# Performance work log

Hardware: AMD Instinct MI355X
Metric: run time of the kernel (lower is better)

Reference implementation:

```python
import jax, jax.numpy as jnp
import numpy as np

D_IN = 768      # inp_dim
NH = 8          # head_num
HD = 96         # head_dim
HID = NH * HD   # 768
UP = 2 * D_IN   # p_factor[0]=2.0 -> 1536
FUSED = 2 * NH + 3 * HID  # 2320
KER = 4
CS = 64         # chunk_size
CAP = 15.0      # gate_soft_cap
EPS = 1e-6


def _ln(x, w, b):
    m = jnp.mean(x, -1, keepdims=True)
    v = jnp.mean((x - m) ** 2, -1, keepdims=True)
    return (x - m) / jnp.sqrt(v + EPS) * w + b


def setup_inputs() -> dict:
    key = jax.random.key(0)
    ks = jax.random.split(key, 10)
    B, S = 2, 4096
    def lin(k, fin, fout):
        return (jax.random.normal(k, (fin, fout), jnp.float32) / np.sqrt(fin)).astype(jnp.float32)
    return {
        "x": jax.random.normal(ks[0], (B, S, D_IN), jnp.float32),
        "ln_in_w": jnp.ones((D_IN,), jnp.float32), "ln_in_b": jnp.zeros((D_IN,), jnp.float32),
        "ln_hid_w": jnp.ones((HID,), jnp.float32), "ln_hid_b": jnp.zeros((HID,), jnp.float32),
        "up_l_w": lin(ks[1], D_IN, UP), "up_l_b": jnp.zeros((UP,), jnp.float32),
        "up_r_w": lin(ks[2], D_IN, HID), "up_r_b": jnp.zeros((HID,), jnp.float32),
        "down_w": lin(ks[3], HID, D_IN), "down_b": jnp.zeros((D_IN,), jnp.float32),
        "conv_w": (jax.random.normal(ks[4], (KER,), jnp.float32) * 0.5).astype(jnp.float32),
        "conv_b": jnp.zeros((), jnp.float32),
        "skip_w": lin(ks[5], UP, HID), "skip_b": jnp.zeros((HID,), jnp.float32),
        "fused_w": lin(ks[6], UP, FUSED), "fused_b": jnp.zeros((FUSED,), jnp.float32),
        "wo_w": lin(ks[7], UP, HID), "wo_b": jnp.zeros((HID,), jnp.float32),
    }


def reference(x, ln_in_w, ln_in_b, ln_hid_w, ln_hid_b, up_l_w, up_l_b, up_r_w, up_r_b,
              down_w, down_b, conv_w, conv_b, skip_w, skip_b, fused_w, fused_b, wo_w, wo_b):
    B, S, _ = x.shape
    soft_cap = lambda t: CAP * jnp.tanh(t / CAP)

    x_n = _ln(x, ln_in_w, ln_in_b)
    x_t = x_n @ up_l_w + up_l_b          # [B,S,UP]
    r_t = x_n @ up_r_w + up_r_b          # [B,S,HID]

    # causal conv: single shared (1,1,KER) kernel, depthwise across UP channels
    xp = jnp.pad(x_t, ((0, 0), (KER - 1, 0), (0, 0)))
    x_c = conv_b + sum(conv_w[j] * xp[:, j:j + S, :] for j in range(KER))
    x_c = jax.nn.silu(x_c)

    x_skip = x_c @ skip_w + skip_b
    proj = x_c @ fused_w + fused_b
    i_pre = soft_cap(proj[..., :NH])
    f_pre = soft_cap(proj[..., NH:2 * NH])
    q, k, v = jnp.split(proj[..., 2 * NH:], 3, axis=-1)
    o = jax.nn.sigmoid(x_t @ wo_w + wo_b)

    resh = lambda t: t.reshape(B, S, NH, HD).transpose(0, 2, 1, 3)  # [B,NH,S,HD]
    q = resh(q)
    k = resh(k) / np.sqrt(HD)
    v = resh(v)

    i_g = i_pre.transpose(0, 2, 1)  # [B,NH,S]
    f_g = f_pre.transpose(0, 2, 1)
    mx = jnp.maximum(f_g, i_g)
    i_g = jnp.exp(i_g - mx)
    f_g = jnp.exp(f_g - mx)

    NC = S // CS
    qc = q.reshape(B, NH, NC, CS, HD)
    kc = k.reshape(B, NH, NC, CS, HD)
    vc = v.reshape(B, NH, NC, CS, HD)
    ic = i_g.reshape(B, NH, NC, CS)
    fc = f_g.reshape(B, NH, NC, CS)

    lf = jnp.cumsum(jnp.log(fc + 1e-8), -1)          # [B,NH,NC,CS]
    f_cumul = jnp.exp(lf - lf[..., -1:])
    wC = f_cumul * ic
    # inter-chunk states; final_forget = exp(lf[-1]-lf[-1]) == 1 exactly -> exclusive cumsum
    C_contrib = jnp.einsum('bncl,bncld,bncle->bncde', wC, vc, kc)  # v-outer-k
    n_contrib = jnp.einsum('bncl,bncld->bncd', wC, kc)
    C_init = jnp.concatenate([jnp.zeros_like(C_contrib[:, :, :1]),
                              jnp.cumsum(C_contrib, axis=2)[:, :, :-1]], axis=2)
    n_init = jnp.concatenate([jnp.zeros_like(n_contrib[:, :, :1]),
                              jnp.cumsum(n_contrib, axis=2)[:, :, :-1]], axis=2)

    # intra-chunk, strictly-causal (j < i)
    mask = jnp.tril(jnp.ones((CS, CS), bool), -1)
    dl = lf[..., :, None] - lf[..., None, :]
    w = jnp.where(mask, ic[..., None, :] * jnp.exp(jnp.where(mask, dl, 0.0)), 0.0)
    scores = jnp.einsum('bncid,bncjd->bncij', qc, kc)
    attn = jax.nn.softmax(jnp.where(mask, scores, -1e30), axis=-1)
    attn = jnp.where(mask, attn, 0.0)  # pos 0 row -> all zeros

    h_intra = jnp.einsum('bncij,bncjd->bncid', attn * w, vc)
    n_intra = jnp.einsum('bncij,bncjd->bncid', w, kc)
    h_init = jnp.einsum('bncde,bncie->bncid', C_init, qc)

    total_n = n_init[..., None, :] + n_intra
    denom = jnp.maximum(jnp.sum(total_n * qc, -1, keepdims=True), 1.0)
    h = (h_init + h_intra) / denom                    # [B,NH,NC,CS,HD]

    h = h.reshape(B, NH, S, HD).transpose(0, 2, 1, 3).reshape(B, S, HID)
    h = o * h
    out = _ln(h, ln_hid_w, ln_hid_b) + x_skip
    out = out * jax.nn.silu(r_t)
    out = out @ down_w + down_b
    return out + x
```

## Files before the change

kernel.cpp:

```cpp
#include <hip/hip_runtime.h>
#include <hip/hip_bf16.h>
#include <math.h>

#define D_IN  768
#define NHD   8
#define HDIM  96
#define HID   768
#define UPD   1536
#define FUSED 2320
#define KER   4
#define CS    64
#define NCH   64
#define SB    4096
#define BB    2
#define NROW  (BB*SB)
#define NCHUNK (BB*NHD*NCH)

using u16   = unsigned short;
using frag8 = __attribute__((ext_vector_type(8))) short;
using f32x4 = __attribute__((ext_vector_type(4))) float;

#define O_WUPL   0
#define O_WUPR   1769472
#define O_WSKIP  2359296
#define O_WFUS   3538944
#define O_WWO    9142272
#define O_WDOWN  10321920
#define O_RT     10911744
#define O_XSKIP  17203200
#define O_LF     23494656
#define O_IC     23560192
#define O_WC     23625728
#define O_NC     23691264
#define O_XN     23789568
#define O_XT     33226752
#define O_XTS    45809664
#define O_PROJ   23789568
#define O_CC     23789568
#define O_H      33226752
#define O_OUT1   39518208

__device__ __forceinline__ void gld_lds16u(const u16* g, u16* l) {
    __builtin_amdgcn_global_load_lds(
        (const __attribute__((address_space(1))) void*)g,
        (__attribute__((address_space(3))) void*)l, 16, 0, 0);
}

__device__ __forceinline__ void split3u(float f, unsigned &H, unsigned &M, unsigned &L) {
    unsigned u = __float_as_uint(f);
    unsigned hr = (u + 0x7fffu + ((u >> 16) & 1u)) & 0xffff0000u;
    H = hr;
    float rm = f - __uint_as_float(hr);
    unsigned mr = __float_as_uint(rm) & 0xffff0000u;
    M = mr;
    float rl = rm - __uint_as_float(mr);
    L = __float_as_uint(rl) & 0xffff0000u;
}

__global__ __launch_bounds__(256) void tpose_split(
    const float* __restrict__ w, u16* __restrict__ tH, u16* __restrict__ tM,
    u16* __restrict__ tL, int K, int N)
{
    __shared__ float tile[64][65];
    int k0 = blockIdx.x * 64, n0 = blockIdx.y * 64;
    int t = threadIdx.x;
    int c = t & 63, r4 = t >> 6;
    #pragma unroll
    for (int it = 0; it < 16; ++it) {
        int r = r4 + it * 4;
        int n = n0 + c;
        tile[r][c] = (n < N) ? w[(size_t)(k0 + r) * N + n] : 0.f;
    }
    __syncthreads();
    #pragma unroll
    for (int it = 0; it < 16; ++it) {
        int nn = r4 + it * 4;
        float v = tile[c][nn];
        unsigned H, M, L;
        split3u(v, H, M, L);
        size_t idx = (size_t)(n0 + nn) * K + k0 + c;
        tH[idx] = (u16)(H >> 16);
        tM[idx] = (u16)(M >> 16);
        if (tL) tL[idx] = (u16)(L >> 16);
    }
}

__global__ __launch_bounds__(256) void ln_in_split(
    const float* __restrict__ x, const float* __restrict__ w,
    const float* __restrict__ b, u16* __restrict__ oH,
    u16* __restrict__ oM, u16* __restrict__ oL)
{
    int row = blockIdx.x;
    size_t base = (size_t)row * D_IN;
    int c0 = threadIdx.x, c1 = threadIdx.x + 256, c2 = threadIdx.x + 512;
    float v0 = x[base + c0], v1 = x[base + c1], v2 = x[base + c2];
    float s = v0 + v1 + v2;
    float ss = v0*v0 + v1*v1 + v2*v2;
    for (int off = 32; off; off >>= 1) { s += __shfl_xor(s, off); ss += __shfl_xor(ss, off); }
    __shared__ float red[8];
    int wid = threadIdx.x >> 6;
    if ((threadIdx.x & 63) == 0) { red[wid] = s; red[4 + wid] = ss; }
    __syncthreads();
    s = red[0] + red[1] + red[2] + red[3];
    ss = red[4] + red[5] + red[6] + red[7];
    float mean = s * (1.f / D_IN);
    float var = ss * (1.f / D_IN) - mean * mean;
    float inv = rsqrtf(var + 1e-6f);
    float r0 = (v0 - mean) * inv * w[c0] + b[c0];
    float r1 = (v1 - mean) * inv * w[c1] + b[c1];
    float r2 = (v2 - mean) * inv * w[c2] + b[c2];
    unsigned H, M, L;
    split3u(r0, H, M, L); oH[base+c0]=(u16)(H>>16); oM[base+c0]=(u16)(M>>16); oL[base+c0]=(u16)(L>>16);
    split3u(r1, H, M, L); oH[base+c1]=(u16)(H>>16); oM[base+c1]=(u16)(M>>16); oL[base+c1]=(u16)(L>>16);
    split3u(r2, H, M, L); oH[base+c2]=(u16)(H>>16); oM[base+c2]=(u16)(M>>16); oL[base+c2]=(u16)(L>>16);
}

template<int NT, int NTH>
__global__ __launch_bounds__(NTH) void gemm_sp(
    const u16* __restrict__ aH, const u16* __restrict__ aM, const u16* __restrict__ aL,
    const u16* __restrict__ bH, const u16* __restrict__ bM, const u16* __restrict__ bL,
    const float* __restrict__ bias, const float* __restrict__ resid,
    float* __restrict__ C, u16* __restrict__ cH, u16* __restrict__ cM,
    int N, int K, int act)
{
    constexpr int BM = (NT == 6) ? 256 : 128;
    __shared__ u16 AHM[2][BM * 64];
    __shared__ u16 BHM[2][128 * 64];
    __shared__ u16 ALp[(NT == 6) ? 2 : 1][(NT == 6) ? 128 * 64 : 8];
    __shared__ u16 BLp[(NT == 6) ? 2 : 1][(NT == 6) ? 64 * 64 : 8];

    int t = threadIdx.x;
    int wave = t >> 6, lane = t & 63;
    int lin = blockIdx.y * gridDim.x + blockIdx.x;
    int cpx = (gridDim.x * gridDim.y) >> 3;
    int sw  = (lin & 7) * cpx + (lin >> 3);
    int bx = sw % gridDim.x, by = sw / gridDim.x;
    int m0 = by * BM, n0 = bx * 128;

    int wm = (wave >> 1) * 64, wn = (wave & 1) * 64;
    f32x4 acc[4][4] = {};

    int l7 = lane & 7, l8 = lane >> 3;
    int lc = l7 ^ l8;
    int lane15 = lane & 15, rsel = lane >> 4;
    int pH = (rsel ^ l7) * 8;
    int pM = ((4 | rsel) ^ l7) * 8;
    int aLrow = (lane15 >> 1) * 64 + (((((lane & 1) << 2) | rsel) ^ (lane15 >> 1)) * 8);
    int wslot = wave;

    auto stage = [&](int buf, int k0) {
        if constexpr (NT == 6) {
            #pragma unroll
            for (int j = 0; j < 4; ++j) {
                int g = j * 8 + wslot;
                int r = g * 8 + l8;
                const u16* src = (lc >= 4 ? aM : aH) + (size_t)(m0 + r) * K + k0 + (lc & 3) * 8;
                gld_lds16u(src, &AHM[buf][g * 512 + lane * 8]);
            }
            #pragma unroll
            for (int j = 0; j < 2; ++j) {
                int g = j * 8 + wslot;
                int r = g * 8 + l8;
                const u16* src = (lc >= 4 ? bM : bH) + (size_t)(n0 + r) * K + k0 + (lc & 3) * 8;
                gld_lds16u(src, &BHM[buf][g * 512 + lane * 8]);
            }
            #pragma unroll
            for (int j = 0; j < 2; ++j) {
                int g = j * 8 + wslot;
                int R = g * 8 + l8;
                int rr = 2 * R + (lc >> 2);
                const u16* src = aL + (size_t)(m0 + rr) * K + k0 + (lc & 3) * 8;
                gld_lds16u(src, &ALp[buf][g * 512 + lane * 8]);
            }
            {
                int g = wslot;
                int R = g * 8 + l8;
                int rr = 2 * R + (lc >> 2);
                const u16* src = bL + (size_t)(n0 + rr) * K + k0 + (lc & 3) * 8;
                gld_lds16u(src, &BLp[buf][g * 512 + lane * 8]);
            }
        } else {
            #pragma unroll
            for (int j = 0; j < 4; ++j) {
                int g = j * 4 + wslot;
                int r = g * 8 + l8;
                const u16* src = (lc >= 4 ? aM : aH) + (size_t)(m0 + r) * K + k0 + (lc & 3) * 8;
                gld_lds16u(src, &AHM[buf][g * 512 + lane * 8]);
            }
            #pragma unroll
            for (int j = 0; j < 4; ++j) {
                int g = j * 4 + wslot;
                int r = g * 8 + l8;
                const u16* src = (lc >= 4 ? bM : bH) + (size_t)(n0 + r) * K + k0 + (lc & 3) * 8;
                gld_lds16u(src, &BHM[buf][g * 512 + lane * 8]);
            }
        }
    };

    auto compute = [&](int buf) {
        frag8 ah[4], am[4], al[(NT == 6) ? 4 : 1];
        #pragma unroll
        for (int mi = 0; mi < 4; ++mi) {
            int rr = wm + mi * 16 + lane15;
            const u16* bp = &AHM[buf][rr * 64];
            ah[mi] = *(const frag8*)&bp[pH];
            am[mi] = *(const frag8*)&bp[pM];
            if constexpr (NT == 6)
                al[mi] = *(const frag8*)&ALp[buf][(wm >> 1) * 64 + mi * 512 + aLrow];
        }
        #pragma unroll
        for (int ni = 0; ni < 4; ++ni) {
            int rb = wn + ni * 16 + lane15;
            const u16* bp = &BHM[buf][rb * 64];
            frag8 bh = *(const frag8*)&bp[pH];
            frag8 bm = *(const frag8*)&bp[pM];
            if constexpr (NT == 6) {
                frag8 bl = *(const frag8*)&BLp[buf][(wn >> 1) * 64 + ni * 512 + aLrow];
                #pragma unroll
                for (int mi = 0; mi < 4; ++mi) {
                    acc[mi][ni] = __builtin_amdgcn_mfma_f32_16x16x32_bf16(ah[mi], bm, acc[mi][ni], 0, 0, 0);
                    acc[mi][ni] = __builtin_amdgcn_mfma_f32_16x16x32_bf16(am[mi], bh, acc[mi][ni], 0, 0, 0);
                    acc[mi][ni] = __builtin_amdgcn_mfma_f32_16x16x32_bf16(ah[mi], bl, acc[mi][ni], 0, 0, 0);
                    acc[mi][ni] = __builtin_amdgcn_mfma_f32_16x16x32_bf16(al[mi], bh, acc[mi][ni], 0, 0, 0);
                    acc[mi][ni] = __builtin_amdgcn_mfma_f32_16x16x32_bf16(am[mi], bm, acc[mi][ni], 0, 0, 0);
                    acc[mi][ni] = __builtin_amdgcn_mfma_f32_16x16x32_bf16(ah[mi], bh, acc[mi][ni], 0, 0, 0);
                }
            } else {
                #pragma unroll
                for (int mi = 0; mi < 4; ++mi) {
                    acc[mi][ni] = __builtin_amdgcn_mfma_f32_16x16x32_bf16(ah[mi], bm, acc[mi][ni], 0, 0, 0);
                    acc[mi][ni] = __builtin_amdgcn_mfma_f32_16x16x32_bf16(am[mi], bh, acc[mi][ni], 0, 0, 0);
                    acc[mi][ni] = __builtin_amdgcn_mfma_f32_16x16x32_bf16(ah[mi], bh, acc[mi][ni], 0, 0, 0);
                }
            }
        }
    };

    int ns = K >> 5;
    stage(0, 0);
    asm volatile("" ::: "memory");
    int cur = 0;
    for (int s = 0; s < ns - 1; ++s) {
        stage(cur ^ 1, (s + 1) * 32);
        if constexpr (NT == 6) asm volatile("s_waitcnt vmcnt(9)" ::: "memory");
        else                   asm volatile("s_waitcnt vmcnt(8)" ::: "memory");
        __builtin_amdgcn_sched_barrier(0);
        __builtin_amdgcn_s_barrier();
        compute(cur);
        __builtin_amdgcn_s_barrier();
        cur ^= 1;
    }
    asm volatile("s_waitcnt vmcnt(0)" ::: "memory");
    __builtin_amdgcn_sched_barrier(0);
    __builtin_amdgcn_s_barrier();
    compute(cur);

    const bool dosplit = (cH != nullptr);
    #pragma unroll
    for (int ni = 0; ni < 4; ++ni) {
        int ncol = n0 + wn + ni * 16 + (lane & 15);
        if (ncol >= N) continue;
        float bs = bias[ncol];
        #pragma unroll
        for (int mi = 0; mi < 4; ++mi) {
            #pragma unroll
            for (int r = 0; r < 4; ++r) {
                int mrow = m0 + wm + mi * 16 + (lane >> 4) * 4 + r;
                float val = acc[mi][ni][r] + bs;
                if (act == 1) val = 1.f / (1.f + expf(-val));
                if (resid) val += resid[(size_t)mrow * N + ncol];
                C[(size_t)mrow * N + ncol] = val;
                if (dosplit) {
                    unsigned H, M, L;
                    split3u(val, H, M, L);
                    cH[(size_t)mrow * N + ncol] = (u16)(H >> 16);
                    cM[(size_t)mrow * N + ncol] = (u16)(M >> 16);
                }
            }
        }
    }
}

__global__ void conv_split(const float* __restrict__ xt, const float* __restrict__ cw,
                           const float* __restrict__ cb, u16* __restrict__ xcH,
                           u16* __restrict__ xcM, u16* __restrict__ xcL)
{
    size_t idx = (size_t)blockIdx.x * blockDim.x + threadIdx.x;
    if (idx >= (size_t)NROW * UPD) return;
    int ch = idx % UPD;
    int s = (int)((idx / UPD) % SB);
    int b = (int)(idx / ((size_t)UPD * SB));
    float acc = cb[0];
    #pragma unroll
    for (int j = 0; j < KER; ++j) {
        int sj = s - (KER - 1) + j;
        if (sj >= 0) acc += cw[j] * xt[((size_t)b * SB + sj) * UPD + ch];
    }
    float v = acc / (1.f + expf(-acc));
    unsigned H, M, L;
    split3u(v, H, M, L);
    xcH[idx] = (u16)(H >> 16);
    xcM[idx] = (u16)(M >> 16);
    xcL[idx] = (u16)(L >> 16);
}

__global__ __launch_bounds__(64) void gates_kernel(
    const float* __restrict__ proj, float* __restrict__ lf,
    float* __restrict__ ic, float* __restrict__ wC)
{
    int cid = blockIdx.x;
    int l = threadIdx.x;
    int b = cid >> 9;
    int nh = (cid >> 6) & 7;
    int c = cid & 63;
    int s = c * CS + l;
    size_t row = ((size_t)b * SB + s) * FUSED;
    float ip = proj[row + nh];
    float fp = proj[row + NHD + nh];
    ip = 15.f * tanhf(ip * (1.f / 15.f));
    fp = 15.f * tanhf(fp * (1.f / 15.f));
    float mx = fmaxf(ip, fp);
    float ig = expf(ip - mx);
    float fg = expf(fp - mx);
    float v = logf(fg + 1e-8f);
    for (int off = 1; off < 64; off <<= 1) {
        float u = __shfl_up(v, off);
        if (l >= off) v += u;
    }
    float last = __shfl(v, 63);
    lf[cid * CS + l] = v;
    ic[cid * CS + l] = ig;
    wC[cid * CS + l] = expf(v - last) * ig;
}

__global__ void repack_kernel(const float* __restrict__ proj, float* __restrict__ q,
                              float* __restrict__ k, float* __restrict__ v)
{
    size_t idx = (size_t)blockIdx.x * blockDim.x + threadIdx.x;
    if (idx >= (size_t)BB * NHD * NCH * CS * HDIM) return;
    int d = idx % HDIM; size_t r1 = idx / HDIM;
    int l = r1 % CS; r1 /= CS;
    int c = r1 % NCH; r1 /= NCH;
    int nh = r1 % NHD; int b = (int)(r1 / NHD);
    size_t row = ((size_t)b * SB + c * CS + l) * FUSED + 2 * NHD + nh * HDIM + d;
    q[idx] = proj[row];
    k[idx] = proj[row + HID] * 0.10206207261596577f;
    v[idx] = proj[row + 2 * HID];
}

__global__ __launch_bounds__(256) void chunk_outer_kernel(
    const float* __restrict__ k, const float* __restrict__ v,
    const float* __restrict__ wC, float* __restrict__ Cc, float* __restrict__ nc)
{
    __shared__ float kL[CS * HDIM], vL[CS * HDIM], wL[CS];
    int cid = blockIdx.x, t = threadIdx.x;
    const float* kg = k + (size_t)cid * CS * HDIM;
    const float* vg = v + (size_t)cid * CS * HDIM;
    for (int idx = t; idx < CS * HDIM; idx += 256) { kL[idx] = kg[idx]; vL[idx] = vg[idx]; }
    if (t < CS) wL[t] = wC[cid * CS + t];
    __syncthreads();
    int eb = t >> 3;
    int db = t & 7;
    float4 acc[3][3];
    #pragma unroll
    for (int e2 = 0; e2 < 3; ++e2)
        #pragma unroll
        for (int x = 0; x < 3; ++x) acc[e2][x] = make_float4(0.f, 0.f, 0.f, 0.f);
    for (int l = 0; l < CS; ++l) {
        float w = wL[l];
        float wk[3];
        #pragma unroll
        for (int e2 = 0; e2 < 3; ++e2) wk[e2] = w * kL[l * HDIM + 3 * eb + e2];
        const float* vr = &vL[l * HDIM + 12 * db];
        float4 vv[3];
        #pragma unroll
        for (int x = 0; x < 3; ++x) vv[x] = *(const float4*)(vr + 4 * x);
        #pragma unroll
        for (int e2 = 0; e2 < 3; ++e2)
            #pragma unroll
            for (int x = 0; x < 3; ++x) {
                acc[e2][x].x += wk[e2] * vv[x].x;
                acc[e2][x].y += wk[e2] * vv[x].y;
                acc[e2][x].z += wk[e2] * vv[x].z;
                acc[e2][x].w += wk[e2] * vv[x].w;
            }
    }
    float* Cb = Cc + (size_t)cid * HDIM * HDIM;
    #pragma unroll
    for (int e2 = 0; e2 < 3; ++e2)
        #pragma unroll
        for (int x = 0; x < 3; ++x)
            *(float4*)&Cb[(size_t)(3 * eb + e2) * HDIM + 12 * db + 4 * x] = acc[e2][x];
    if (t < HDIM) {
        float acc2 = 0.f;
        for (int l = 0; l < CS; ++l) acc2 += wL[l] * kL[l * HDIM + t];
        nc[(size_t)cid * HDIM + t] = acc2;
    }
}

__global__ void scan_kernel(float* __restrict__ Cc, float* __restrict__ nc)
{
    int gid = blockIdx.x * blockDim.x + threadIdx.x;
    const int NCE = BB * NHD * HDIM * HDIM;
    if (gid < NCE) {
        int bh = gid / (HDIM * HDIM);
        int ent = gid % (HDIM * HDIM);
        float run = 0.f;
        float* base = Cc + (size_t)bh * NCH * HDIM * HDIM + ent;
        for (int c = 0; c < NCH; ++c) {
            float tv = base[(size_t)c * HDIM * HDIM];
            base[(size_t)c * HDIM * HDIM] = run;
            run += tv;
        }
    } else {
        int g2 = gid - NCE;
        if (g2 < BB * NHD * HDIM) {
            int bh = g2 / HDIM, ent = g2 % HDIM;
            float run = 0.f;
            float* base = nc + (size_t)bh * NCH * HDIM + ent;
            for (int c = 0; c < NCH; ++c) {
                float tv = base[c * HDIM];
                base[c * HDIM] = run;
                run += tv;
            }
        }
    }
}

__global__ __launch_bounds__(256) void attn_kernel(
    const float* __restrict__ q, const float* __restrict__ k, const float* __restrict__ v,
    const float* __restrict__ lf, const float* __restrict__ ic,
    const float* __restrict__ CiT, const float* __restrict__ ni,
    float* __restrict__ hout)
{
    __shared__ float qL[64 * 100];
    __shared__ float kL[64 * 100];
    __shared__ float lfL[64], icL[64], niL[96], dinvL[64];
    int cid = blockIdx.x, t = threadIdx.x;
    int b = cid >> 9, nh = (cid >> 6) & 7, c = cid & 63;
    const float* qg = q + (size_t)cid * (CS * HDIM);
    const float* kg = k + (size_t)cid * (CS * HDIM);
    const float* vg = v + (size_t)cid * (CS * HDIM);
    const float4* qg4 = (const float4*)qg;
    const float4* kg4 = (const float4*)kg;
    #pragma unroll
    for (int it = 0; it < 6; ++it) {
        int idx = t + it * 256;
        int row = idx / 24, col = (idx % 24) * 4;
        *(float4*)&qL[row * 100 + col] = qg4[idx];
        *(float4*)&kL[row * 100 + col] = kg4[idx];
    }
    if (t < 64) { lfL[t] = lf[cid * CS + t]; icL[t] = ic[cid * CS + t]; }
    else if (t < 160) { niL[t - 64] = ni[(size_t)cid * HDIM + (t - 64)]; }
    __syncthreads();

    int i = t >> 2, g = t & 3;
    const float* qrow = qL + i * 100;
    float sc[16];
    #pragma unroll
    for (int jj = 0; jj < 16; ++jj) sc[jj] = 0.f;
    for (int d4 = 0; d4 < 24; ++d4) {
        float4 qv = *(const float4*)(qrow + 4 * d4);
        #pragma unroll
        for (int jj = 0; jj < 16; ++jj) {
            float4 kv = *(const float4*)(kL + (g + 4 * jj) * 100 + 4 * d4);
            sc[jj] += qv.x * kv.x + qv.y * kv.y + qv.z * kv.z + qv.w * kv.w;
        }
    }
    float lfi = lfL[i];
    float wv[16];
    #pragma unroll
    for (int jj = 0; jj < 16; ++jj) {
        int j = g + 4 * jj;
        wv[jj] = (j < i) ? icL[j] * expf(lfi - lfL[j]) : 0.f;
    }
    float den = 0.f;
    #pragma unroll
    for (int jj = 0; jj < 16; ++jj) den += wv[jj] * sc[jj];
    #pragma unroll
    for (int dd = 0; dd < 24; ++dd) {
        int d = 24 * g + dd;
        den += niL[d] * qrow[d];
    }
    float m = -1e30f;
    #pragma unroll
    for (int jj = 0; jj < 16; ++jj) { int j = g + 4 * jj; if (j < i) m = fmaxf(m, sc[jj]); }
    m = fmaxf(m, __shfl_xor(m, 1)); m = fmaxf(m, __shfl_xor(m, 2));
    float p = 0.f;
    #pragma unroll
    for (int jj = 0; jj < 16; ++jj) {
        int j = g + 4 * jj;
        sc[jj] = (j < i) ? expf(sc[jj] - m) : 0.f;
        p += sc[jj];
    }
    p += __shfl_xor(p, 1); p += __shfl_xor(p, 2);
    float pinv = (p > 0.f) ? 1.f / p : 0.f;
    __syncthreads();
    float* awL = kL;
    #pragma unroll
    for (int jj = 0; jj < 16; ++jj) {
        int j = g + 4 * jj;
        awL[i * 68 + j] = sc[jj] * pinv * wv[jj];
    }
    den += __shfl_xor(den, 1); den += __shfl_xor(den, 2);
    if ((t & 3) == 0) dinvL[i] = 1.f / fmaxf(den, 1.f);
    __syncthreads();

    int i0 = (t >> 3) << 1, db = (t & 7) * 12;
    float4 h4[2][3];
    #pragma unroll
    for (int r = 0; r < 2; ++r)
        #pragma unroll
        for (int x = 0; x < 3; ++x) h4[r][x] = make_float4(0.f, 0.f, 0.f, 0.f);
    const float* vb = vg + db;
    const float* aw0 = awL + i0 * 68;
    for (int j = 0; j < 64; ++j) {
        float a0 = aw0[j];
        float a1 = aw0[68 + j];
        const float4* vr = (const float4*)(vb + j * HDIM);
        #pragma unroll
        for (int x = 0; x < 3; ++x) {
            float4 vv = vr[x];
            h4[0][x].x += a0 * vv.x; h4[0][x].y += a0 * vv.y;
            h4[0][x].z += a0 * vv.z; h4[0][x].w += a0 * vv.w;
            h4[1][x].x += a1 * vv.x; h4[1][x].y += a1 * vv.y;
            h4[1][x].z += a1 * vv.z; h4[1][x].w += a1 * vv.w;
        }
    }
    const float* Cb = CiT + (size_t)cid * (HDIM * HDIM) + db;
    const float* qr0 = qL + i0 * 100;
    const float* qr1 = qr0 + 100;
    for (int e = 0; e < 96; ++e) {
        float q0 = qr0[e], q1 = qr1[e];
        const float4* cr = (const float4*)(Cb + e * HDIM);
        #pragma unroll
        for (int x = 0; x < 3; ++x) {
            float4 cv = cr[x];
            h4[0][x].x += q0 * cv.x; h4[0][x].y += q0 * cv.y;
            h4[0][x].z += q0 * cv.z; h4[0][x].w += q0 * cv.w;
            h4[1][x].x += q1 * cv.x; h4[1][x].y += q1 * cv.y;
            h4[1][x].z += q1 * cv.z; h4[1][x].w += q1 * cv.w;
        }
    }
    float di0 = dinvL[i0], di1 = dinvL[i0 + 1];
    int s0 = c * CS + i0;
    float4* hr0 = (float4*)(hout + (((size_t)b * SB + s0) * NHD + nh) * HDIM + db);
    float4* hr1 = (float4*)(hout + (((size_t)b * SB + s0 + 1) * NHD + nh) * HDIM + db);
    #pragma unroll
    for (int x = 0; x < 3; ++x) {
        float4 h0 = h4[0][x], h1 = h4[1][x];
        h0.x *= di0; h0.y *= di0; h0.z *= di0; h0.w *= di0;
        h1.x *= di1; h1.y *= di1; h1.z *= di1; h1.w *= di1;
        hr0[x] = h0;
        hr1[x] = h1;
    }
}

__global__ __launch_bounds__(256) void ln_hid_split(
    const float* __restrict__ h, const float* __restrict__ o,
    const float* __restrict__ xskip, const float* __restrict__ rt,
    const float* __restrict__ w, const float* __restrict__ bb,
    u16* __restrict__ oH, u16* __restrict__ oM)
{
    int row = blockIdx.x;
    size_t base = (size_t)row * HID;
    int c0 = threadIdx.x, c1 = threadIdx.x + 256, c2 = threadIdx.x + 512;
    float v0 = o[base + c0] * h[base + c0];
    float v1 = o[base + c1] * h[base + c1];
    float v2 = o[base + c2] * h[base + c2];
    float s = v0 + v1 + v2;
    float ss = v0*v0 + v1*v1 + v2*v2;
    for (int off = 32; off; off >>= 1) { s += __shfl_xor(s, off); ss += __shfl_xor(ss, off); }
    __shared__ float red[8];
    int wid = threadIdx.x >> 6;
    if ((threadIdx.x & 63) == 0) { red[wid] = s; red[4 + wid] = ss; }
    __syncthreads();
    s = red[0] + red[1] + red[2] + red[3];
    ss = red[4] + red[5] + red[6] + red[7];
    float mean = s * (1.f / HID);
    float var = ss * (1.f / HID) - mean * mean;
    float inv = rsqrtf(var + 1e-6f);
    float g0 = rt[base + c0], g1 = rt[base + c1], g2 = rt[base + c2];
    float r0 = ((v0 - mean) * inv * w[c0] + bb[c0] + xskip[base + c0]) * (g0 / (1.f + expf(-g0)));
    float r1 = ((v1 - mean) * inv * w[c1] + bb[c1] + xskip[base + c1]) * (g1 / (1.f + expf(-g1)));
    float r2 = ((v2 - mean) * inv * w[c2] + bb[c2] + xskip[base + c2]) * (g2 / (1.f + expf(-g2)));
    unsigned H, M, L;
    split3u(r0, H, M, L); oH[base+c0]=(u16)(H>>16); oM[base+c0]=(u16)(M>>16);
    split3u(r1, H, M, L); oH[base+c1]=(u16)(H>>16); oM[base+c1]=(u16)(M>>16);
    split3u(r2, H, M, L); oH[base+c2]=(u16)(H>>16); oM[base+c2]=(u16)(M>>16);
}

extern "C" void kernel_launch(void* const* d_in, const int* in_sizes, int n_in,
                              void* d_out, int out_size, void* d_ws, size_t ws_size,
                              hipStream_t stream)
{
    const float* x       = (const float*)d_in[0];
    const float* ln_in_w = (const float*)d_in[1];
    const float* ln_in_b = (const float*)d_in[2];
    const float* ln_hid_w= (const float*)d_in[3];
    const float* ln_hid_b= (const float*)d_in[4];
    const float* up_l_w  = (const float*)d_in[5];
    const float* up_l_b  = (const float*)d_in[6];
    const float* up_r_w  = (const float*)d_in[7];
    const float* up_r_b  = (const float*)d_in[8];
    const float* down_w  = (const float*)d_in[9];
    const float* down_b  = (const float*)d_in[10];
    const float* conv_w  = (const float*)d_in[11];
    const float* conv_b  = (const float*)d_in[12];
    const float* skip_w  = (const float*)d_in[13];
    const float* skip_b  = (const float*)d_in[14];
    const float* fused_w = (const float*)d_in[15];
    const float* fused_b = (const float*)d_in[16];
    const float* wo_w    = (const float*)d_in[17];
    const float* wo_b    = (const float*)d_in[18];
    float* out = (float*)d_out;

    float* ws = (float*)d_ws;
    u16* wuplH = (u16*)(ws + O_WUPL);  u16* wuplM = wuplH + 1179648; u16* wuplL = wuplM + 1179648;
    u16* wuprH = (u16*)(ws + O_WUPR);  u16* wuprM = wuprH + 589824;
    u16* wskpH = (u16*)(ws + O_WSKIP); u16* wskpM = wskpH + 1179648;
    u16* wfusH = (u16*)(ws + O_WFUS);  u16* wfusM = wfusH + 3735552; u16* wfusL = wfusM + 3735552;
    u16* wwoH  = (u16*)(ws + O_WWO);   u16* wwoM  = wwoH  + 1179648;
    u16* wdwnH = (u16*)(ws + O_WDOWN); u16* wdwnM = wdwnH + 589824;
    float* rt    = ws + O_RT;
    float* xskip = ws + O_XSKIP;
    float* lf    = ws + O_LF;
    float* ic    = ws + O_IC;
    float* wC    = ws + O_WC;
    float* nc    = ws + O_NC;
    u16* xnH = (u16*)(ws + O_XN);  u16* xnM = xnH + 6291456; u16* xnL = xnM + 6291456;
    float* xt = ws + O_XT;
    u16* xtH = (u16*)(ws + O_XTS); u16* xtM = xtH + 12582912;
    u16* xcH = (u16*)(ws + O_XTS); u16* xcM = xcH + 12582912; u16* xcL = xcM + 12582912;
    float* proj = ws + O_PROJ;
    float* q = ws + O_XTS;
    float* k = ws + O_XTS + 6291456;
    float* v = ws + O_XTS + 12582912;
    float* Cc = ws + O_CC;
    float* h  = ws + O_H;
    u16* out1H = (u16*)(ws + O_OUT1); u16* out1M = out1H + 6291456;
    float* o = (float*)d_out;

    tpose_split<<<dim3(12, 24), 256, 0, stream>>>(up_l_w, wuplH, wuplM, wuplL, 768, 1536);
    tpose_split<<<dim3(12, 12), 256, 0, stream>>>(up_r_w, wuprH, wuprM, nullptr, 768, 768);
    tpose_split<<<dim3(24, 12), 256, 0, stream>>>(skip_w, wskpH, wskpM, nullptr, 1536, 768);
    tpose_split<<<dim3(24, 38), 256, 0, stream>>>(fused_w, wfusH, wfusM, wfusL, 1536, 2320);
    tpose_split<<<dim3(24, 12), 256, 0, stream>>>(wo_w, wwoH, wwoM, nullptr, 1536, 768);
    tpose_split<<<dim3(12, 12), 256, 0, stream>>>(down_w, wdwnH, wdwnM, nullptr, 768, 768);
    ln_in_split<<<NROW, 256, 0, stream>>>(x, ln_in_w, ln_in_b, xnH, xnM, xnL);
    gemm_sp<6,512><<<dim3(12, 32), 512, 0, stream>>>(xnH, xnM, xnL, wuplH, wuplM, wuplL,
        up_l_b, nullptr, xt, xtH, xtM, UPD, D_IN, 0);
    gemm_sp<3,256><<<dim3(6, 64), 256, 0, stream>>>(xnH, xnM, nullptr, wuprH, wuprM, nullptr,
        up_r_b, nullptr, rt, nullptr, nullptr, HID, D_IN, 0);
    gemm_sp<3,256><<<dim3(6, 64), 256, 0, stream>>>(xtH, xtM, nullptr, wwoH, wwoM, nullptr,
        wo_b, nullptr, o, nullptr, nullptr, HID, UPD, 1);
    {
        size_t tot = (size_t)NROW * UPD;
        conv_split<<<(unsigned)((tot + 255) / 256), 256, 0, stream>>>(xt, conv_w, conv_b, xcH, xcM, xcL);
    }
    gemm_sp<3,256><<<dim3(6, 64), 256, 0, stream>>>(xcH, xcM, nullptr, wskpH, wskpM, nullptr,
        skip_b, nullptr, xskip, nullptr, nullptr, HID, UPD, 0);
    gemm_sp<6,512><<<dim3(19, 32), 512, 0, stream>>>(xcH, xcM, xcL, wfusH, wfusM, wfusL,
        fused_b, nullptr, proj, nullptr, nullptr, FUSED, UPD, 0);
    gates_kernel<<<NCHUNK, 64, 0, stream>>>(proj, lf, ic, wC);
    {
        size_t tot = (size_t)BB * NHD * NCH * CS * HDIM;
        repack_kernel<<<(unsigned)((tot + 255) / 256), 256, 0, stream>>>(proj, q, k, v);
    }
    chunk_outer_kernel<<<NCHUNK, 256, 0, stream>>>(k, v, wC, Cc, nc);
    {
        int tot = BB * NHD * HDIM * HDIM + BB * NHD * HDIM;
        scan_kernel<<<(tot + 255) / 256, 256, 0, stream>>>(Cc, nc);
    }
    attn_kernel<<<NCHUNK, 256, 0, stream>>>(q, k, v, lf, ic, Cc, nc, h);
    ln_hid_split<<<NROW, 256, 0, stream>>>(h, o, xskip, rt, ln_hid_w, ln_hid_b, out1H, out1M);
    gemm_sp<3,256><<<dim3(6, 64), 256, 0, stream>>>(out1H, out1M, nullptr, wdwnH, wdwnM, nullptr,
        down_b, x, out, nullptr, nullptr, D_IN, HID, 0);
}
```

Measured before the change: 1.129 ms.

## Merge sibling GEMMs into mixed-precision launches and drop q/k/v repack kernel

Concatenates up_l and up_r weights into one GEMM launch, and fused and skip weights into another. Tiles in the second region skip the low-order split terms and run 3 MFMAs instead of 6, and their results go to a separate output buffer. The repack kernel is removed, and chunk_outer and attn now read q/k/v directly from proj with strided rows, applying the k scale inline. This cuts launch count and a full copy of q/k/v through memory, in exchange for uncoalesced strided reads from proj and a more complex GEMM epilogue.

```diff
diff --git a/kernel.cpp b/kernel.cpp
--- a/kernel.cpp
+++ b/kernel.cpp
@@ -15,17 +15,16 @@
 #define BB    2
 #define NROW  (BB*SB)
 #define NCHUNK (BB*NHD*NCH)
+#define KSCALE 0.10206207261596577f
 
 using u16   = unsigned short;
 using frag8 = __attribute__((ext_vector_type(8))) short;
 using f32x4 = __attribute__((ext_vector_type(4))) float;
 
-#define O_WUPL   0
-#define O_WUPR   1769472
-#define O_WSKIP  2359296
-#define O_WFUS   3538944
-#define O_WWO    9142272
-#define O_WDOWN  10321920
+#define O_WUP    0
+#define O_WWO    2359296
+#define O_WDOWN  3538944
+#define O_WFUS   4128768
 #define O_RT     10911744
 #define O_XSKIP  17203200
 #define O_LF     23494656
@@ -36,8 +35,8 @@
 #define O_XT     33226752
 #define O_XTS    45809664
 #define O_PROJ   23789568
-#define O_CC     23789568
-#define O_H      33226752
+#define O_CC     45809664
+#define O_H      55246848
 #define O_OUT1   39518208
 
 __device__ __forceinline__ void gld_lds16u(const u16* g, u16* l) {
@@ -121,7 +120,8 @@
     const u16* __restrict__ bH, const u16* __restrict__ bM, const u16* __restrict__ bL,
     const float* __restrict__ bias, const float* __restrict__ resid,
     float* __restrict__ C, u16* __restrict__ cH, u16* __restrict__ cM,
-    int N, int K, int act)
+    int ldC, int N1, int NP1, float* __restrict__ C2, const float* __restrict__ bias2,
+    int K, int act)
 {
     constexpr int BM = (NT == 6) ? 256 : 128;
     __shared__ u16 AHM[2][BM * 64];
@@ -136,6 +136,7 @@
     int sw  = (lin & 7) * cpx + (lin >> 3);
     int bx = sw % gridDim.x, by = sw / gridDim.x;
     int m0 = by * BM, n0 = bx * 128;
+    const bool lact = (NT == 6) && (n0 < NP1);
 
     int wm = (wave >> 1) * 64, wn = (wave & 1) * 64;
     f32x4 acc[4][4] = {};
@@ -164,20 +165,22 @@
                 const u16* src = (lc >= 4 ? bM : bH) + (size_t)(n0 + r) * K + k0 + (lc & 3) * 8;
                 gld_lds16u(src, &BHM[buf][g * 512 + lane * 8]);
             }
-            #pragma unroll
-            for (int j = 0; j < 2; ++j) {
-                int g = j * 8 + wslot;
-                int R = g * 8 + l8;
-                int rr = 2 * R + (lc >> 2);
-                const u16* src = aL + (size_t)(m0 + rr) * K + k0 + (lc & 3) * 8;
-                gld_lds16u(src, &ALp[buf][g * 512 + lane * 8]);
-            }
-            {
-                int g = wslot;
-                int R = g * 8 + l8;
-                int rr = 2 * R + (lc >> 2);
-                const u16* src = bL + (size_t)(n0 + rr) * K + k0 + (lc & 3) * 8;
-                gld_lds16u(src, &BLp[buf][g * 512 + lane * 8]);
+            if (lact) {
+                #pragma unroll
+                for (int j = 0; j < 2; ++j) {
+                    int g = j * 8 + wslot;
+                    int R = g * 8 + l8;
+                    int rr = 2 * R + (lc >> 2);
+                    const u16* src = aL + (size_t)(m0 + rr) * K + k0 + (lc & 3) * 8;
+                    gld_lds16u(src, &ALp[buf][g * 512 + lane * 8]);
+                }
+                {
+                    int g = wslot;
+                    int R = g * 8 + l8;
+                    int rr = 2 * R + (lc >> 2);
+                    const u16* src = bL + (size_t)(n0 + rr) * K + k0 + (lc & 3) * 8;
+                    gld_lds16u(src, &BLp[buf][g * 512 + lane * 8]);
+                }
             }
         } else {
             #pragma unroll
@@ -206,7 +209,7 @@
             ah[mi] = *(const frag8*)&bp[pH];
             am[mi] = *(const frag8*)&bp[pM];
             if constexpr (NT == 6)
-                al[mi] = *(const frag8*)&ALp[buf][(wm >> 1) * 64 + mi * 512 + aLrow];
+                if (lact) al[mi] = *(const frag8*)&ALp[buf][(wm >> 1) * 64 + mi * 512 + aLrow];
         }
         #pragma unroll
         for (int ni = 0; ni < 4; ++ni) {
@@ -215,15 +218,24 @@
             frag8 bh = *(const frag8*)&bp[pH];
             frag8 bm = *(const frag8*)&bp[pM];
             if constexpr (NT == 6) {
-                frag8 bl = *(const frag8*)&BLp[buf][(wn >> 1) * 64 + ni * 512 + aLrow];
-                #pragma unroll
-                for (int mi = 0; mi < 4; ++mi) {
-                    acc[mi][ni] = __builtin_amdgcn_mfma_f32_16x16x32_bf16(ah[mi], bm, acc[mi][ni], 0, 0, 0);
-                    acc[mi][ni] = __builtin_amdgcn_mfma_f32_16x16x32_bf16(am[mi], bh, acc[mi][ni], 0, 0, 0);
-                    acc[mi][ni] = __builtin_amdgcn_mfma_f32_16x16x32_bf16(ah[mi], bl, acc[mi][ni], 0, 0, 0);
-                    acc[mi][ni] = __builtin_amdgcn_mfma_f32_16x16x32_bf16(al[mi], bh, acc[mi][ni], 0, 0, 0);
-                    acc[mi][ni] = __builtin_amdgcn_mfma_f32_16x16x32_bf16(am[mi], bm, acc[mi][ni], 0, 0, 0);
-                    acc[mi][ni] = __builtin_amdgcn_mfma_f32_16x16x32_bf16(ah[mi], bh, acc[mi][ni], 0, 0, 0);
+                if (lact) {
+                    frag8 bl = *(const frag8*)&BLp[buf][(wn >> 1) * 64 + ni * 512 + aLrow];
+                    #pragma unroll
+                    for (int mi = 0; mi < 4; ++mi) {
+                        acc[mi][ni] = __builtin_amdgcn_mfma_f32_16x16x32_bf16(ah[mi], bm, acc[mi][ni], 0, 0, 0);
+                        acc[mi][ni] = __builtin_amdgcn_mfma_f32_16x16x32_bf16(am[mi], bh, acc[mi][ni], 0, 0, 0);
+                        acc[mi][ni] = __builtin_amdgcn_mfma_f32_16x16x32_bf16(ah[mi], bl, acc[mi][ni], 0, 0, 0);
+                        acc[mi][ni] = __builtin_amdgcn_mfma_f32_16x16x32_bf16(al[mi], bh, acc[mi][ni], 0, 0, 0);
+                        acc[mi][ni] = __builtin_amdgcn_mfma_f32_16x16x32_bf16(am[mi], bm, acc[mi][ni], 0, 0, 0);
+                        acc[mi][ni] = __builtin_amdgcn_mfma_f32_16x16x32_bf16(ah[mi], bh, acc[mi][ni], 0, 0, 0);
+                    }
+                } else {
+                    #pragma unroll
+                    for (int mi = 0; mi < 4; ++mi) {
+                        acc[mi][ni] = __builtin_amdgcn_mfma_f32_16x16x32_bf16(ah[mi], bm, acc[mi][ni], 0, 0, 0);
+                        acc[mi][ni] = __builtin_amdgcn_mfma_f32_16x16x32_bf16(am[mi], bh, acc[mi][ni], 0, 0, 0);
+                        acc[mi][ni] = __builtin_amdgcn_mfma_f32_16x16x32_bf16(ah[mi], bh, acc[mi][ni], 0, 0, 0);
+                    }
                 }
             } else {
                 #pragma unroll
@@ -242,8 +254,12 @@
     int cur = 0;
     for (int s = 0; s < ns - 1; ++s) {
         stage(cur ^ 1, (s + 1) * 32);
-        if constexpr (NT == 6) asm volatile("s_waitcnt vmcnt(9)" ::: "memory");
-        else                   asm volatile("s_waitcnt vmcnt(8)" ::: "memory");
+        if constexpr (NT == 6) {
+            if (lact) asm volatile("s_waitcnt vmcnt(9)" ::: "memory");
+            else      asm volatile("s_waitcnt vmcnt(6)" ::: "memory");
+        } else {
+            asm volatile("s_waitcnt vmcnt(8)" ::: "memory");
+        }
         __builtin_amdgcn_sched_barrier(0);
         __builtin_amdgcn_s_barrier();
         compute(cur);
@@ -259,8 +275,12 @@
     #pragma unroll
     for (int ni = 0; ni < 4; ++ni) {
         int ncol = n0 + wn + ni * 16 + (lane & 15);
-        if (ncol >= N) continue;
-        float bs = bias[ncol];
+        bool r1 = (ncol < N1);
+        float* Cp; int ld, cc;
+        if (r1) { Cp = C; ld = ldC; cc = ncol; }
+        else if (C2 != nullptr && ncol >= NP1) { Cp = C2; ld = 768; cc = ncol - NP1; }
+        else continue;
+        float bs = r1 ? bias[ncol] : bias2[cc];
         #pragma unroll
         for (int mi = 0; mi < 4; ++mi) {
             #pragma unroll
@@ -268,13 +288,13 @@
                 int mrow = m0 + wm + mi * 16 + (lane >> 4) * 4 + r;
                 float val = acc[mi][ni][r] + bs;
                 if (act == 1) val = 1.f / (1.f + expf(-val));
-                if (resid) val += resid[(size_t)mrow * N + ncol];
-                C[(size_t)mrow * N + ncol] = val;
-                if (dosplit) {
+                if (resid && r1) val += resid[(size_t)mrow * ld + cc];
+                Cp[(size_t)mrow * ld + cc] = val;
+                if (dosplit && r1) {
                     unsigned H, M, L;
                     split3u(val, H, M, L);
-                    cH[(size_t)mrow * N + ncol] = (u16)(H >> 16);
-                    cM[(size_t)mrow * N + ncol] = (u16)(M >> 16);
+                    cH[(size_t)mrow * ld + cc] = (u16)(H >> 16);
+                    cM[(size_t)mrow * ld + cc] = (u16)(M >> 16);
                 }
             }
         }
@@ -333,30 +353,19 @@
     wC[cid * CS + l] = expf(v - last) * ig;
 }
 
-__global__ void repack_kernel(const float* __restrict__ proj, float* __restrict__ q,
-                              float* __restrict__ k, float* __restrict__ v)
-{
-    size_t idx = (size_t)blockIdx.x * blockDim.x + threadIdx.x;
-    if (idx >= (size_t)BB * NHD * NCH * CS * HDIM) return;
-    int d = idx % HDIM; size_t r1 = idx / HDIM;
-    int l = r1 % CS; r1 /= CS;
-    int c = r1 % NCH; r1 /= NCH;
-    int nh = r1 % NHD; int b = (int)(r1 / NHD);
-    size_t row = ((size_t)b * SB + c * CS + l) * FUSED + 2 * NHD + nh * HDIM + d;
-    q[idx] = proj[row];
-    k[idx] = proj[row + HID] * 0.10206207261596577f;
-    v[idx] = proj[row + 2 * HID];
-}
-
 __global__ __launch_bounds__(256) void chunk_outer_kernel(
-    const float* __restrict__ k, const float* __restrict__ v,
-    const float* __restrict__ wC, float* __restrict__ Cc, float* __restrict__ nc)
+    const float* __restrict__ proj, const float* __restrict__ wC,
+    float* __restrict__ Cc, float* __restrict__ nc)
 {
     __shared__ float kL[CS * HDIM], vL[CS * HDIM], wL[CS];
     int cid = blockIdx.x, t = threadIdx.x;
-    const float* kg = k + (size_t)cid * CS * HDIM;
-    const float* vg = v + (size_t)cid * CS * HDIM;
-    for (int idx = t; idx < CS * HDIM; idx += 256) { kL[idx] = kg[idx]; vL[idx] = vg[idx]; }
+    int b = cid >> 9, nh = (cid >> 6) & 7, c = cid & 63;
+    const float* pg = proj + ((size_t)b * SB + (size_t)c * CS) * FUSED + 2 * NHD + nh * HDIM;
+    for (int idx = t; idx < CS * HDIM; idx += 256) {
+        int row = idx / HDIM, col = idx - row * HDIM;
+        kL[idx] = pg[(size_t)row * FUSED + HID + col] * KSCALE;
+        vL[idx] = pg[(size_t)row * FUSED + 2 * HID + col];
+    }
     if (t < CS) wL[t] = wC[cid * CS + t];
     __syncthreads();
     int eb = t >> 3;
@@ -428,8 +437,7 @@
 }
 
 __global__ __launch_bounds__(256) void attn_kernel(
-    const float* __restrict__ q, const float* __restrict__ k, const float* __restrict__ v,
-    const float* __restrict__ lf, const float* __restrict__ ic,
+    const float* __restrict__ proj, const float* __restrict__ lf, const float* __restrict__ ic,
     const float* __restrict__ CiT, const float* __restrict__ ni,
     float* __restrict__ hout)
 {
@@ -438,17 +446,17 @@
     __shared__ float lfL[64], icL[64], niL[96], dinvL[64];
     int cid = blockIdx.x, t = threadIdx.x;
     int b = cid >> 9, nh = (cid >> 6) & 7, c = cid & 63;
-    const float* qg = q + (size_t)cid * (CS * HDIM);
-    const float* kg = k + (size_t)cid * (CS * HDIM);
-    const float* vg = v + (size_t)cid * (CS * HDIM);
-    const float4* qg4 = (const float4*)qg;
-    const float4* kg4 = (const float4*)kg;
+    const float* pq = proj + ((size_t)b * SB + (size_t)c * CS) * FUSED + 2 * NHD + nh * HDIM;
+    const float* pk = pq + HID;
+    const float* pv = pq + 2 * HID;
     #pragma unroll
     for (int it = 0; it < 6; ++it) {
         int idx = t + it * 256;
         int row = idx / 24, col = (idx % 24) * 4;
-        *(float4*)&qL[row * 100 + col] = qg4[idx];
-        *(float4*)&kL[row * 100 + col] = kg4[idx];
+        *(float4*)&qL[row * 100 + col] = *(const float4*)(pq + (size_t)row * FUSED + col);
+        float4 kv = *(const float4*)(pk + (size_t)row * FUSED + col);
+        kv.x *= KSCALE; kv.y *= KSCALE; kv.z *= KSCALE; kv.w *= KSCALE;
+        *(float4*)&kL[row * 100 + col] = kv;
     }
     if (t < 64) { lfL[t] = lf[cid * CS + t]; icL[t] = ic[cid * CS + t]; }
     else if (t < 160) { niL[t - 64] = ni[(size_t)cid * HDIM + (t - 64)]; }
@@ -512,12 +520,12 @@
     for (int r = 0; r < 2; ++r)
         #pragma unroll
         for (int x = 0; x < 3; ++x) h4[r][x] = make_float4(0.f, 0.f, 0.f, 0.f);
-    const float* vb = vg + db;
+    const float* vb = pv + db;
     const float* aw0 = awL + i0 * 68;
     for (int j = 0; j < 64; ++j) {
         float a0 = aw0[j];
         float a1 = aw0[68 + j];
-        const float4* vr = (const float4*)(vb + j * HDIM);
+        const float4* vr = (const float4*)(vb + (size_t)j * FUSED);
         #pragma unroll
         for (int x = 0; x < 3; ++x) {
             float4 vv = vr[x];
@@ -616,12 +624,10 @@
     float* out = (float*)d_out;
 
     float* ws = (float*)d_ws;
-    u16* wuplH = (u16*)(ws + O_WUPL);  u16* wuplM = wuplH + 1179648; u16* wuplL = wuplM + 1179648;
-    u16* wuprH = (u16*)(ws + O_WUPR);  u16* wuprM = wuprH + 589824;
-    u16* wskpH = (u16*)(ws + O_WSKIP); u16* wskpM = wskpH + 1179648;
-    u16* wfusH = (u16*)(ws + O_WFUS);  u16* wfusM = wfusH + 3735552; u16* wfusL = wfusM + 3735552;
+    u16* wupH = (u16*)(ws + O_WUP);    u16* wupM = wupH + 1769472; u16* wupL = wupM + 1769472;
     u16* wwoH  = (u16*)(ws + O_WWO);   u16* wwoM  = wwoH  + 1179648;
     u16* wdwnH = (u16*)(ws + O_WDOWN); u16* wdwnM = wdwnH + 589824;
+    u16* wfusH = (u16*)(ws + O_WFUS);  u16* wfusM = wfusH + 4915200; u16* wfusL = wfusM + 4915200;
     float* rt    = ws + O_RT;
     float* xskip = ws + O_XSKIP;
     float* lf    = ws + O_LF;
@@ -633,47 +639,36 @@
     u16* xtH = (u16*)(ws + O_XTS); u16* xtM = xtH + 12582912;
     u16* xcH = (u16*)(ws + O_XTS); u16* xcM = xcH + 12582912; u16* xcL = xcM + 12582912;
     float* proj = ws + O_PROJ;
-    float* q = ws + O_XTS;
-    float* k = ws + O_XTS + 6291456;
-    float* v = ws + O_XTS + 12582912;
     float* Cc = ws + O_CC;
     float* h  = ws + O_H;
     u16* out1H = (u16*)(ws + O_OUT1); u16* out1M = out1H + 6291456;
     float* o = (float*)d_out;
 
-    tpose_split<<<dim3(12, 24), 256, 0, stream>>>(up_l_w, wuplH, wuplM, wuplL, 768, 1536);
-    tpose_split<<<dim3(12, 12), 256, 0, stream>>>(up_r_w, wuprH, wuprM, nullptr, 768, 768);
-    tpose_split<<<dim3(24, 12), 256, 0, stream>>>(skip_w, wskpH, wskpM, nullptr, 1536, 768);
+    tpose_split<<<dim3(12, 24), 256, 0, stream>>>(up_l_w, wupH, wupM, wupL, 768, 1536);
+    tpose_split<<<dim3(12, 12), 256, 0, stream>>>(up_r_w, wupH + 1179648, wupM + 1179648, nullptr, 768, 768);
     tpose_split<<<dim3(24, 38), 256, 0, stream>>>(fused_w, wfusH, wfusM, wfusL, 1536, 2320);
+    tpose_split<<<dim3(24, 12), 256, 0, stream>>>(skip_w, wfusH + 3735552, wfusM + 3735552, nullptr, 1536, 768);
     tpose_split<<<dim3(24, 12), 256, 0, stream>>>(wo_w, wwoH, wwoM, nullptr, 1536, 768);
     tpose_split<<<dim3(12, 12), 256, 0, stream>>>(down_w, wdwnH, wdwnM, nullptr, 768, 768);
     ln_in_split<<<NROW, 256, 0, stream>>>(x, ln_in_w, ln_in_b, xnH, xnM, xnL);
-    gemm_sp<6,512><<<dim3(12, 32), 512, 0, stream>>>(xnH, xnM, xnL, wuplH, wuplM, wuplL,
-        up_l_b, nullptr, xt, xtH, xtM, UPD, D_IN, 0);
-    gemm_sp<3,256><<<dim3(6, 64), 256, 0, stream>>>(xnH, xnM, nullptr, wuprH, wuprM, nullptr,
-        up_r_b, nullptr, rt, nullptr, nullptr, HID, D_IN, 0);
+    gemm_sp<6,512><<<dim3(18, 32), 512, 0, stream>>>(xnH, xnM, xnL, wupH, wupM, wupL,
+        up_l_b, nullptr, xt, xtH, xtM, UPD, UPD, UPD, rt, up_r_b, D_IN, 0);
     gemm_sp<3,256><<<dim3(6, 64), 256, 0, stream>>>(xtH, xtM, nullptr, wwoH, wwoM, nullptr,
-        wo_b, nullptr, o, nullptr, nullptr, HID, UPD, 1);
+        wo_b, nullptr, o, nullptr, nullptr, HID, HID, 1 << 30, nullptr, nullptr, UPD, 1);
     {
         size_t tot = (size_t)NROW * UPD;
         conv_split<<<(unsigned)((tot + 255) / 256), 256, 0, stream>>>(xt, conv_w, conv_b, xcH, xcM, xcL);
     }
-    gemm_sp<3,256><<<dim3(6, 64), 256, 0, stream>>>(xcH, xcM, nullptr, wskpH, wskpM, nullptr,
-        skip_b, nullptr, xskip, nullptr, nullptr, HID, UPD, 0);
-    gemm_sp<6,512><<<dim3(19, 32), 512, 0, stream>>>(xcH, xcM, xcL, wfusH, wfusM, wfusL,
-        fused_b, nullptr, proj, nullptr, nullptr, FUSED, UPD, 0);
+    gemm_sp<6,512><<<dim3(25, 32), 512, 0, stream>>>(xcH, xcM, xcL, wfusH, wfusM, wfusL,
+        fused_b, nullptr, proj, nullptr, nullptr, FUSED, FUSED, 2432, xskip, skip_b, UPD, 0);
     gates_kernel<<<NCHUNK, 64, 0, stream>>>(proj, lf, ic, wC);
-    {
-        size_t tot = (size_t)BB * NHD * NCH * CS * HDIM;
-        repack_kernel<<<(unsigned)((tot + 255) / 256), 256, 0, stream>>>(proj, q, k, v);
-    }
-    chunk_outer_kernel<<<NCHUNK, 256, 0, stream>>>(k, v, wC, Cc, nc);
+    chunk_outer_kernel<<<NCHUNK, 256, 0, stream>>>(proj, wC, Cc, nc);
     {
         int tot = BB * NHD * HDIM * HDIM + BB * NHD * HDIM;
         scan_kernel<<<(tot + 255) / 256, 256, 0, stream>>>(Cc, nc);
     }
-    attn_kernel<<<NCHUNK, 256, 0, stream>>>(q, k, v, lf, ic, Cc, nc, h);
+    attn_kernel<<<NCHUNK, 256, 0, stream>>>(proj, lf, ic, Cc, nc, h);
     ln_hid_split<<<NROW, 256, 0, stream>>>(h, o, xskip, rt, ln_hid_w, ln_hid_b, out1H, out1M);
     gemm_sp<3,256><<<dim3(6, 64), 256, 0, stream>>>(out1H, out1M, nullptr, wdwnH, wdwnM, nullptr,
-        down_b, x, out, nullptr, nullptr, D_IN, HID, 0);
-}
+        down_b, x, out, nullptr, nullptr, D_IN, D_IN, 1 << 30, nullptr, nullptr, HID, 0);
+}
```

Result: slower. 1.177 ms (+4.2%).
